# Kernel tuning notes

Hardware: AMD Instinct MI355X
Metric: run time of the kernel (lower is better)

Reference implementation:

```python
import jax, jax.numpy as jnp
import numpy as np

B, S, D, K, F = 4, 2048, 1024, 4, 4096
C_COEF = 8.0  # RG-LRU gating exponent from Griffin paper
EPS = 1e-6


def setup_inputs() -> dict:
    key = jax.random.key(0)
    ks = jax.random.split(key, 12)
    def n(k, shape, scale=1.0):
        return jax.random.normal(k, shape, dtype=jnp.float32) * scale
    sd = 1.0 / np.sqrt(D)
    return {
        "x": n(ks[0], (B, S, D)),
        "velocity": n(ks[1], (B, S, D), 0.1),
        "pre_norm_w": jnp.ones((D,), jnp.float32),
        "conv_kernel": n(ks[2], (D, K), 0.3),   # depthwise causal conv weights
        "conv_bias": jnp.zeros((D,), jnp.float32),
        "W_gate": n(ks[3], (D, D), sd),
        "W_a": n(ks[4], (D, D), sd),
        "lam": n(ks[5], (D,)),
        "W_out": n(ks[6], (2 * D, D), 1.0 / np.sqrt(2 * D)),
        "b_out": jnp.zeros((D,), jnp.float32),
        "log_beta": n(ks[7], (D,), 0.5),
        "ffn_norm_w": jnp.ones((D,), jnp.float32),
        "W_ff1": n(ks[8], (D, F), sd),
        "b_ff1": jnp.zeros((F,), jnp.float32),
        "W_ff2": n(ks[9], (F, D), 1.0 / np.sqrt(F)),
        "b_ff2": jnp.zeros((D,), jnp.float32),
    }


def _rmsnorm(x, w):
    # matches: rsqrt(x.float().pow(2).mean(-1, keepdim=True) + 1e-6); cast back; * weight
    xf = x.astype(jnp.float32)
    rms = jax.lax.rsqrt(jnp.mean(xf * xf, axis=-1, keepdims=True) + EPS)
    return (xf * rms).astype(x.dtype) * w


def _causal_dwconv(x, kernel, bias):
    # y[b,t,d] = bias[d] + sum_k kernel[d,k] * x[b,t-k,d]  (causal depthwise)
    k_taps = kernel.shape[1]
    s = x.shape[1]
    pad = jnp.pad(x, ((0, 0), (k_taps - 1, 0), (0, 0)))
    out = bias
    for k in range(k_taps):  # tiny fixed loop over kernel taps
        out = out + pad[:, k_taps - 1 - k : k_taps - 1 - k + s, :] * kernel[:, k]
    return out


def _griffin_scan(x, W_gate, W_a, lam):
    # RG-LRU: h_t = a_t * h_{t-1} + sqrt(1 - a_t^2) * (i_t * x_t)
    gate = jax.nn.sigmoid(jnp.einsum("bsd,de->bse", x, W_gate))
    log_a = -C_COEF * jax.nn.softplus(lam) * jax.nn.sigmoid(
        jnp.einsum("bsd,de->bse", x, W_a)
    )  # [B,S,D], log_a <= 0
    a = jnp.exp(log_a)
    u = jnp.sqrt(jnp.maximum(1.0 - a * a, 0.0)) * (gate * x)

    def step(h, au):
        a_t, u_t = au
        h = a_t * h + u_t
        return h, h

    a_t = jnp.moveaxis(a, 1, 0)  # [S,B,D]
    u_t = jnp.moveaxis(u, 1, 0)
    h0 = jnp.zeros_like(a_t[0])
    _, hs = jax.lax.scan(step, h0, (a_t, u_t))
    return jnp.moveaxis(hs, 0, 1)  # [B,S,D]


def reference(x, velocity, pre_norm_w, conv_kernel, conv_bias, W_gate, W_a, lam,
              W_out, b_out, log_beta, ffn_norm_w, W_ff1, b_ff1, W_ff2, b_ff2):
    x_norm = _rmsnorm(x, pre_norm_w)
    conv_out = _causal_dwconv(x_norm, conv_kernel, conv_bias)
    griffin_out = _griffin_scan(x_norm, W_gate, W_a, lam)
    mixer_out = jnp.concatenate([conv_out, griffin_out], axis=-1) @ W_out + b_out
    beta = jax.nn.sigmoid(log_beta)
    velocity = beta * velocity + mixer_out
    x = x + velocity
    normed = _rmsnorm(x, ffn_norm_w)
    ffn = jax.nn.gelu(normed @ W_ff1 + b_ff1) @ W_ff2 + b_ff2
    return (x + ffn, velocity)
```

## Files before the change

### kernel.cpp

```cpp
#include <hip/hip_runtime.h>

static constexpr int Bb = 4;
static constexpr int Ss = 2048;
static constexpr int Dd = 1024;
static constexpr int Ff = 4096;
static constexpr int Mm = Bb * Ss;
static constexpr size_t ND = (size_t)Mm * Dd;
static constexpr int CH = 32;
static constexpr int CL = Ss / CH;

typedef __attribute__((ext_vector_type(8))) short short8;
typedef __attribute__((ext_vector_type(4))) float floatx4;

__device__ __forceinline__ unsigned f2bf(float f) {
  unsigned u = __builtin_bit_cast(unsigned, f);
  return (u + 0x7FFFu + ((u >> 16) & 1u)) >> 16;
}
__device__ __forceinline__ float bf2f(unsigned bits) {
  return __builtin_bit_cast(float, bits << 16);
}
__device__ __forceinline__ void gload_lds16(const void* g, void* lds) {
  __builtin_amdgcn_global_load_lds((const __attribute__((address_space(1))) void*)g,
                                   (__attribute__((address_space(3))) void*)lds,
                                   16, 0, 0);
}
__device__ __forceinline__ float fsig(float x) {
  return __builtin_amdgcn_rcpf(1.0f + __expf(-x));
}
__device__ __forceinline__ float fgelu(float v) {
  float z = 1.5957691216057308f * fmaf(0.044715f * v, v * v, v);
  return v * __builtin_amdgcn_rcpf(1.0f + __expf(-z));
}

__global__ __launch_bounds__(256) void wconv_k(const float* __restrict__ W,
                                               unsigned short* __restrict__ WT,
                                               int K, int N) {
  __shared__ float tile[32][33];
  int tx = threadIdx.x & 31, ty = threadIdx.x >> 5;
  int bx = blockIdx.x * 32, by = blockIdx.y * 32;
#pragma unroll
  for (int i = 0; i < 32; i += 8)
    tile[ty + i][tx] = W[(size_t)(by + ty + i) * N + bx + tx];
  __syncthreads();
#pragma unroll
  for (int i = 0; i < 32; i += 8)
    WT[(size_t)(bx + ty + i) * K + by + tx] = (unsigned short)f2bf(tile[tx][ty + i]);
}

__global__ __launch_bounds__(256) void rmsnorm_bf_k(const float* __restrict__ x,
                                                    const float* __restrict__ w,
                                                    unsigned short* __restrict__ out) {
  int row = blockIdx.x;
  const float4* xr = (const float4*)(x + (size_t)row * Dd);
  int t = threadIdx.x;
  float4 v = xr[t];
  float ss = v.x * v.x + v.y * v.y + v.z * v.z + v.w * v.w;
#pragma unroll
  for (int off = 32; off > 0; off >>= 1) ss += __shfl_down(ss, off, 64);
  __shared__ float sb[4];
  if ((t & 63) == 0) sb[t >> 6] = ss;
  __syncthreads();
  float tot = sb[0] + sb[1] + sb[2] + sb[3];
  float sc = rsqrtf(tot * (1.0f / (float)Dd) + 1e-6f);
  float4 wv = ((const float4*)w)[t];
  unsigned lo = f2bf(v.x * sc * wv.x) | (f2bf(v.y * sc * wv.y) << 16);
  unsigned hi = f2bf(v.z * sc * wv.z) | (f2bf(v.w * sc * wv.w) << 16);
  *(uint2*)(out + (size_t)row * Dd + t * 4) = make_uint2(lo, hi);
}

__global__ __launch_bounds__(256) void conv_k(const unsigned short* __restrict__ xn,
                                              const float* __restrict__ kern,
                                              const float* __restrict__ bias,
                                              unsigned short* __restrict__ outC) {
  size_t q = (size_t)blockIdx.x * 256 + threadIdx.x;
  size_t i = q * 4;
  int d = (int)(i & (Dd - 1));
  int m = (int)(i >> 10);
  int t = m & (Ss - 1);
  float acc[4];
#pragma unroll
  for (int j = 0; j < 4; j++) acc[j] = bias[d + j];
#pragma unroll
  for (int k = 0; k < 4; k++) {
    if (t >= k) {
      uint2 xv = *(const uint2*)(xn + i - (size_t)k * Dd);
      float x0 = bf2f(xv.x & 0xFFFF), x1 = bf2f(xv.x >> 16);
      float x2 = bf2f(xv.y & 0xFFFF), x3 = bf2f(xv.y >> 16);
      acc[0] = fmaf(kern[(d + 0) * 4 + k], x0, acc[0]);
      acc[1] = fmaf(kern[(d + 1) * 4 + k], x1, acc[1]);
      acc[2] = fmaf(kern[(d + 2) * 4 + k], x2, acc[2]);
      acc[3] = fmaf(kern[(d + 3) * 4 + k], x3, acc[3]);
    }
  }
  unsigned lo = f2bf(acc[0]) | (f2bf(acc[1]) << 16);
  unsigned hi = f2bf(acc[2]) | (f2bf(acc[3]) << 16);
  *(uint2*)(outC + (size_t)m * (2 * Dd) + d) = make_uint2(lo, hi);
}

template <int MODE>
__global__ __launch_bounds__(512, 2) void bgemm3_k(const unsigned short* __restrict__ A,
                                                   const unsigned short* __restrict__ BT,
                                                   void* __restrict__ Cout,
                                                   int M, int N, int K,
                                                   const float* __restrict__ bias,
                                                   const float* __restrict__ extra,
                                                   const float* __restrict__ vel_in,
                                                   const float* __restrict__ x_in,
                                                   const float* __restrict__ log_beta,
                                                   float* __restrict__ vel_out) {
  __shared__ unsigned short LA[2][256 * 64];
  __shared__ unsigned short LB[2][256 * 64];
  const int tid = threadIdx.x;
  const int wid = tid >> 6, lane = tid & 63;
  const int wm = wid >> 2, wn = wid & 3;
  const int r = lane & 15, quad = lane >> 4, r7 = lane & 7;

  const int gx = gridDim.x;
  int id = blockIdx.y * gx + blockIdx.x;
  const int nwg = gx * gridDim.y;
  id = (id & 7) * (nwg >> 3) + (id >> 3);
  const int bm = (id / gx) * 256, bn = (id % gx) * 256;
  const int NIT = K >> 7;

  const int lrow = lane >> 3;
  const int sblk = (lane & 7) ^ lrow;
  const unsigned short* AsrcB = A  + (size_t)(bm + lrow) * K + sblk * 8;
  const unsigned short* BsrcB = BT + (size_t)(bn + lrow) * K + sblk * 8;

  const int aB = wm * 8192 + r * 64;
  const int bB = wn * 4096 + r * 64;
  const int kq0 = (quad ^ r7) * 8;
  const int kq1 = ((4 + quad) ^ r7) * 8;

  floatx4 acc[8][4];
#pragma unroll
  for (int i = 0; i < 8; i++)
#pragma unroll
    for (int j = 0; j < 4; j++) acc[i][j] = (floatx4){0.f, 0.f, 0.f, 0.f};

#define STG_A(bq, k0, h, s)                                                           \
  gload_lds16(AsrcB + (size_t)((h) * 128 + (s) * 64 + wid * 8) * K + (k0),            \
              (void*)&LA[bq][((h) * 128 + (s) * 64 + wid * 8) * 64])
#define STG_B(bq, k0, h, s)                                                           \
  gload_lds16(BsrcB + (size_t)((h) * 128 + (s) * 64 + wid * 8) * K + (k0),            \
              (void*)&LB[bq][((h) * 128 + (s) * 64 + wid * 8) * 64])
#define RDA(il, IH, buf)                                                              \
  aF[il][0] = *(const short8*)&LA[buf][aB + (IH) * 4096 + (il) * 1024 + kq0];         \
  aF[il][1] = *(const short8*)&LA[buf][aB + (IH) * 4096 + (il) * 1024 + kq1]
#define RDB(BF, jl, jg, buf)                                                          \
  BF[jl][0] = *(const short8*)&LB[buf][bB + (jg) * 1024 + kq0];                       \
  BF[jl][1] = *(const short8*)&LB[buf][bB + (jg) * 1024 + kq1]
#define MM2(il, jl, BF, IH, JH)                                                       \
  acc[(IH) * 4 + (il)][(JH) * 2 + (jl)] = __builtin_amdgcn_mfma_f32_16x16x32_bf16(    \
      BF[jl][0], aF[il][0], acc[(IH) * 4 + (il)][(JH) * 2 + (jl)], 0, 0, 0);          \
  acc[(IH) * 4 + (il)][(JH) * 2 + (jl)] = __builtin_amdgcn_mfma_f32_16x16x32_bf16(    \
      BF[jl][1], aF[il][1], acc[(IH) * 4 + (il)][(JH) * 2 + (jl)], 0, 0, 0)
#define MQUAD(BF, IH, JH)                                                             \
  MM2(0, 0, BF, IH, JH); MM2(0, 1, BF, IH, JH); MM2(1, 0, BF, IH, JH);                \
  MM2(1, 1, BF, IH, JH); MM2(2, 0, BF, IH, JH); MM2(2, 1, BF, IH, JH);                \
  MM2(3, 0, BF, IH, JH); MM2(3, 1, BF, IH, JH)
#define BAR() __builtin_amdgcn_s_barrier()
#define LGK0()                                                                        \
  asm volatile("s_waitcnt lgkmcnt(0)" ::: "memory");                                  \
  __builtin_amdgcn_sched_barrier(0)
#define PRIO(x) __builtin_amdgcn_s_setprio(x)

  STG_A(0, 0, 0, 0); STG_A(0, 0, 0, 1); STG_A(0, 0, 1, 0); STG_A(0, 0, 1, 1);
  STG_B(0, 0, 0, 0); STG_B(0, 0, 0, 1); STG_B(0, 0, 1, 0); STG_B(0, 0, 1, 1);
  STG_B(1, 64, 0, 0); STG_B(1, 64, 0, 1); STG_B(1, 64, 1, 0); STG_B(1, 64, 1, 1);
  asm volatile("s_waitcnt vmcnt(4)" ::: "memory");
  BAR();
  __builtin_amdgcn_sched_barrier(0);

  for (int it = 0; it < NIT; ++it) {
    const int T = 2 * it;
    const int pf = (it + 1 < NIT);
    const int kA1 = (T + 1) << 6;
    const int k2 = (T + 2) << 6, k3 = (T + 3) << 6;
    short8 aF[4][2], b0[2][2], b1[2][2];

    STG_A(1, kA1, 0, 0); STG_A(1, kA1, 0, 1);
    RDA(0, 0, 0); RDA(1, 0, 0); RDA(2, 0, 0); RDA(3, 0, 0);
    RDB(b0, 0, 0, 0); RDB(b0, 1, 1, 0);
    BAR(); LGK0();
    PRIO(1); MQUAD(b0, 0, 0); PRIO(0);
    BAR();

    STG_A(1, kA1, 1, 0); STG_A(1, kA1, 1, 1);
    RDB(b1, 0, 2, 0); RDB(b1, 1, 3, 0);
    BAR(); LGK0();
    PRIO(1); MQUAD(b1, 0, 1); PRIO(0);
    BAR();

    if (pf) { STG_B(0, k2, 0, 0); STG_B(0, k2, 0, 1); }
    RDA(0, 1, 0); RDA(1, 1, 0); RDA(2, 1, 0); RDA(3, 1, 0);
    BAR(); LGK0();
    PRIO(1); MQUAD(b0, 1, 0); PRIO(0);
    BAR();

    if (pf) { STG_B(0, k2, 1, 0); STG_B(0, k2, 1, 1); }
    BAR();
    PRIO(1); MQUAD(b1, 1, 1); PRIO(0);
    if (pf) asm volatile("s_waitcnt vmcnt(4)" ::: "memory");
    else    asm volatile("s_waitcnt vmcnt(0)" ::: "memory");
    BAR();
    __builtin_amdgcn_sched_barrier(0);

    if (pf) { STG_A(0, k2, 0, 0); STG_A(0, k2, 0, 1); }
    RDA(0, 0, 1); RDA(1, 0, 1); RDA(2, 0, 1); RDA(3, 0, 1);
    RDB(b0, 0, 0, 1); RDB(b0, 1, 1, 1);
    BAR(); LGK0();
    PRIO(1); MQUAD(b0, 0, 0); PRIO(0);
    BAR();

    if (pf) { STG_A(0, k2, 1, 0); STG_A(0, k2, 1, 1); }
    RDB(b1, 0, 2, 1); RDB(b1, 1, 3, 1);
    BAR(); LGK0();
    PRIO(1); MQUAD(b1, 0, 1); PRIO(0);
    BAR();

    if (pf) { STG_B(1, k3, 0, 0); STG_B(1, k3, 0, 1); }
    RDA(0, 1, 1); RDA(1, 1, 1); RDA(2, 1, 1); RDA(3, 1, 1);
    BAR(); LGK0();
    PRIO(1); MQUAD(b0, 1, 0); PRIO(0);
    BAR();

    if (pf) { STG_B(1, k3, 1, 0); STG_B(1, k3, 1, 1); }
    BAR();
    PRIO(1); MQUAD(b1, 1, 1); PRIO(0);
    if (pf) {
      asm volatile("s_waitcnt vmcnt(4)" ::: "memory");
      BAR();
      __builtin_amdgcn_sched_barrier(0);
    }
  }
#undef STG_A
#undef STG_B
#undef RDA
#undef RDB
#undef MM2
#undef MQUAD

#pragma unroll
  for (int i = 0; i < 8; i++) {
    int rowg = bm + wm * 128 + i * 16 + r;
#pragma unroll
    for (int j = 0; j < 4; j++) {
      int colg = bn + wn * 64 + j * 16 + quad * 4;
      size_t idx = (size_t)rowg * N + colg;
      float v0 = acc[i][j][0], v1 = acc[i][j][1], v2 = acc[i][j][2], v3 = acc[i][j][3];
      if (MODE & 1) {
        float4 bv = *(const float4*)(bias + colg);
        v0 += bv.x; v1 += bv.y; v2 += bv.z; v3 += bv.w;
      }
      if (MODE & 2) {
        v0 = fgelu(v0); v1 = fgelu(v1); v2 = fgelu(v2); v3 = fgelu(v3);
      }
      if (MODE & 4) {
        float4 ev = *(const float4*)(extra + idx);
        v0 += ev.x; v1 += ev.y; v2 += ev.z; v3 += ev.w;
      }
      if (MODE & 16) {
        float4 lb = *(const float4*)(log_beta + colg);
        float4 vi = *(const float4*)(vel_in + idx);
        float4 xi = *(const float4*)(x_in + idx);
        float4 vn;
        vn.x = fmaf(fsig(lb.x), vi.x, v0);
        vn.y = fmaf(fsig(lb.y), vi.y, v1);
        vn.z = fmaf(fsig(lb.z), vi.z, v2);
        vn.w = fmaf(fsig(lb.w), vi.w, v3);
        *(float4*)(vel_out + idx) = vn;
        v0 = xi.x + vn.x; v1 = xi.y + vn.y; v2 = xi.z + vn.z; v3 = xi.w + vn.w;
      }
      if (MODE & 8) {
        uint2 pk;
        pk.x = f2bf(v0) | (f2bf(v1) << 16);
        pk.y = f2bf(v2) | (f2bf(v3) << 16);
        *(uint2*)((unsigned short*)Cout + idx) = pk;
      } else {
        float4 o; o.x = v0; o.y = v1; o.z = v2; o.w = v3;
        *(float4*)((float*)Cout + idx) = o;
      }
    }
  }
}

template <int MODE>
__global__ __launch_bounds__(512, 2) void bgemm4_k(const unsigned short* __restrict__ A,
                                                   const unsigned short* __restrict__ BT,
                                                   void* __restrict__ Cout,
                                                   int M, int N, int K,
                                                   const float* __restrict__ bias,
                                                   const float* __restrict__ extra,
                                                   const float* __restrict__ vel_in,
                                                   const float* __restrict__ x_in,
                                                   const float* __restrict__ log_beta,
                                                   float* __restrict__ vel_out) {
  __shared__ unsigned short LA[3][256 * 64];
  __shared__ unsigned short LB[2][128 * 64];
  const int tid = threadIdx.x;
  const int wid = tid >> 6, lane = tid & 63;
  const int wm = wid >> 1, wn = wid & 1;
  const int r = lane & 15, quad = lane >> 4, r7 = lane & 7;

  const int gx = gridDim.x;
  int id = blockIdx.y * gx + blockIdx.x;
  const int nwg = gx * gridDim.y;
  id = (id & 7) * (nwg >> 3) + (id >> 3);
  const int bm = (id / gx) * 256, bn = (id % gx) * 128;
  const int NIT = K >> 7;

  const int lrow = lane >> 3;
  const int sblk = (lane & 7) ^ lrow;
  const unsigned short* AsrcB = A  + (size_t)(bm + lrow) * K + sblk * 8;
  const unsigned short* BsrcB = BT + (size_t)(bn + lrow) * K + sblk * 8;

  unsigned short* a0 = &LA[0][0];
  unsigned short* a1 = &LA[1][0];
  unsigned short* a2 = &LA[2][0];
  unsigned short* B0 = &LB[0][0];
  unsigned short* B1 = &LB[1][0];

  const int aB = wm * 4096 + r * 64;
  const int bB = wn * 4096 + r * 64;
  const int kq0 = (quad ^ r7) * 8;
  const int kq1 = ((4 + quad) ^ r7) * 8;

  floatx4 acc[4][4];
#pragma unroll
  for (int i = 0; i < 4; i++)
#pragma unroll
    for (int j = 0; j < 4; j++) acc[i][j] = (floatx4){0.f, 0.f, 0.f, 0.f};

#define STG_A7(dst, k0, h, s)                                                         \
  gload_lds16(AsrcB + (size_t)((h) * 128 + (s) * 64 + wid * 8) * K + (k0),            \
              (void*)((dst) + ((h) * 128 + (s) * 64 + wid * 8) * 64))
#define STG_B7(dst, k0, s)                                                            \
  gload_lds16(BsrcB + (size_t)((s) * 64 + wid * 8) * K + (k0),                        \
              (void*)((dst) + ((s) * 64 + wid * 8) * 64))
#define RDA7(src, IH)                                                                 \
  aF[0][0] = *(const short8*)((src) + aB + (IH) * 2048 + kq0);                        \
  aF[0][1] = *(const short8*)((src) + aB + (IH) * 2048 + kq1);                        \
  aF[1][0] = *(const short8*)((src) + aB + (IH) * 2048 + 1024 + kq0);                 \
  aF[1][1] = *(const short8*)((src) + aB + (IH) * 2048 + 1024 + kq1)
#define RDB7(BF, src, JH)                                                             \
  BF[0][0] = *(const short8*)((src) + bB + (JH) * 2048 + kq0);                        \
  BF[0][1] = *(const short8*)((src) + bB + (JH) * 2048 + kq1);                        \
  BF[1][0] = *(const short8*)((src) + bB + (JH) * 2048 + 1024 + kq0);                 \
  BF[1][1] = *(const short8*)((src) + bB + (JH) * 2048 + 1024 + kq1)
#define MM27(il, jl, BF, IH, JH)                                                      \
  acc[(IH) * 2 + (il)][(JH) * 2 + (jl)] = __builtin_amdgcn_mfma_f32_16x16x32_bf16(    \
      BF[jl][0], aF[il][0], acc[(IH) * 2 + (il)][(JH) * 2 + (jl)], 0, 0, 0);          \
  acc[(IH) * 2 + (il)][(JH) * 2 + (jl)] = __builtin_amdgcn_mfma_f32_16x16x32_bf16(    \
      BF[jl][1], aF[il][1], acc[(IH) * 2 + (il)][(JH) * 2 + (jl)], 0, 0, 0)
#define MQ7(BF, IH, JH)                                                               \
  MM27(0, 0, BF, IH, JH); MM27(0, 1, BF, IH, JH);                                     \
  MM27(1, 0, BF, IH, JH); MM27(1, 1, BF, IH, JH)

  STG_A7(a0, 0, 0, 0); STG_A7(a0, 0, 0, 1); STG_A7(a0, 0, 1, 0); STG_A7(a0, 0, 1, 1);
  STG_B7(B0, 0, 0); STG_B7(B0, 0, 1);
  STG_A7(a1, 64, 0, 0); STG_A7(a1, 64, 0, 1); STG_A7(a1, 64, 1, 0); STG_A7(a1, 64, 1, 1);
  STG_B7(B1, 64, 0); STG_B7(B1, 64, 1);
  asm volatile("s_waitcnt vmcnt(6)" ::: "memory");
  BAR();
  __builtin_amdgcn_sched_barrier(0);

  for (int it = 0; it < NIT; ++it) {
    const int T = 2 * it;
    const int pf = (it + 1 < NIT);
    const int k2 = (T + 2) << 6, k3 = (T + 3) << 6;
    short8 aF[2][2], b0f[2][2], b1f[2][2];

    if (pf) { STG_A7(a2, k2, 0, 0); STG_A7(a2, k2, 0, 1); }
    RDA7(a0, 0); RDB7(b0f, B0, 0);
    BAR(); LGK0();
    PRIO(1); MQ7(b0f, 0, 0); PRIO(0);
    BAR();

    if (pf) { STG_A7(a2, k2, 1, 0); STG_A7(a2, k2, 1, 1); }
    RDB7(b1f, B0, 1);
    BAR(); LGK0();
    PRIO(1); MQ7(b1f, 0, 1); PRIO(0);
    BAR();

    if (pf) STG_B7(B0, k2, 0);
    RDA7(a0, 1);
    BAR(); LGK0();
    PRIO(1); MQ7(b0f, 1, 0); PRIO(0);
    BAR();

    if (pf) STG_B7(B0, k2, 1);
    BAR();
    PRIO(1); MQ7(b1f, 1, 1); PRIO(0);
    if (pf) asm volatile("s_waitcnt vmcnt(6)" ::: "memory");
    else    asm volatile("s_waitcnt vmcnt(0)" ::: "memory");
    BAR();
    __builtin_amdgcn_sched_barrier(0);

    if (pf) { STG_A7(a0, k3, 0, 0); STG_A7(a0, k3, 0, 1); }
    RDA7(a1, 0); RDB7(b0f, B1, 0);
    BAR(); LGK0();
    PRIO(1); MQ7(b0f, 0, 0); PRIO(0);
    BAR();

    if (pf) { STG_A7(a0, k3, 1, 0); STG_A7(a0, k3, 1, 1); }
    RDB7(b1f, B1, 1);
    BAR(); LGK0();
    PRIO(1); MQ7(b1f, 0, 1); PRIO(0);
    BAR();

    if (pf) STG_B7(B1, k3, 0);
    RDA7(a1, 1);
    BAR(); LGK0();
    PRIO(1); MQ7(b0f, 1, 0); PRIO(0);
    BAR();

    if (pf) STG_B7(B1, k3, 1);
    BAR();
    PRIO(1); MQ7(b1f, 1, 1); PRIO(0);
    if (pf) {
      asm volatile("s_waitcnt vmcnt(6)" ::: "memory");
      BAR();
      __builtin_amdgcn_sched_barrier(0);
    }

    unsigned short* tmp = a2; a2 = a1; a1 = a0; a0 = tmp;
  }
#undef STG_A7
#undef STG_B7
#undef RDA7
#undef RDB7
#undef MM27
#undef MQ7
#undef BAR
#undef LGK0
#undef PRIO

#pragma unroll
  for (int i = 0; i < 4; i++) {
    int rowg = bm + wm * 64 + i * 16 + r;
#pragma unroll
    for (int j = 0; j < 4; j++) {
      int colg = bn + wn * 64 + j * 16 + quad * 4;
      size_t idx = (size_t)rowg * N + colg;
      float v0 = acc[i][j][0], v1 = acc[i][j][1], v2 = acc[i][j][2], v3 = acc[i][j][3];
      if (MODE & 1) {
        float4 bv = *(const float4*)(bias + colg);
        v0 += bv.x; v1 += bv.y; v2 += bv.z; v3 += bv.w;
      }
      if (MODE & 2) {
        v0 = fgelu(v0); v1 = fgelu(v1); v2 = fgelu(v2); v3 = fgelu(v3);
      }
      if (MODE & 4) {
        float4 ev = *(const float4*)(extra + idx);
        v0 += ev.x; v1 += ev.y; v2 += ev.z; v3 += ev.w;
      }
      if (MODE & 16) {
        float4 lb = *(const float4*)(log_beta + colg);
        float4 vi = *(const float4*)(vel_in + idx);
        float4 xi = *(const float4*)(x_in + idx);
        float4 vn;
        vn.x = fmaf(fsig(lb.x), vi.x, v0);
        vn.y = fmaf(fsig(lb.y), vi.y, v1);
        vn.z = fmaf(fsig(lb.z), vi.z, v2);
        vn.w = fmaf(fsig(lb.w), vi.w, v3);
        *(float4*)(vel_out + idx) = vn;
        v0 = xi.x + vn.x; v1 = xi.y + vn.y; v2 = xi.z + vn.z; v3 = xi.w + vn.w;
      }
      if (MODE & 8) {
        uint2 pk;
        pk.x = f2bf(v0) | (f2bf(v1) << 16);
        pk.y = f2bf(v2) | (f2bf(v3) << 16);
        *(uint2*)((unsigned short*)Cout + idx) = pk;
      } else {
        float4 o; o.x = v0; o.y = v1; o.z = v2; o.w = v3;
        *(float4*)((float*)Cout + idx) = o;
      }
    }
  }
}

__global__ __launch_bounds__(256) void scan_p1(const unsigned short* __restrict__ gapre,
                                               const unsigned short* __restrict__ xn,
                                               const float* __restrict__ lam,
                                               unsigned short* __restrict__ ub,
                                               float* __restrict__ carryA,
                                               float* __restrict__ carryH) {
  int g = blockIdx.x * 256 + threadIdx.x;
  int e = g & (Dd - 1);
  int bc = g >> 10;
  int b = bc & 3;
  int c = bc >> 2;
  float l = lam[e];
  float sp = fmaxf(l, 0.0f) + log1pf(__expf(-fabsf(l)));
  float m8sp = -8.0f * sp;
  size_t m0 = (size_t)b * Ss + (size_t)c * CL;
  float A = 1.0f, h = 0.0f;
#pragma unroll 4
  for (int t = 0; t < CL; t++) {
    size_t m = m0 + t;
    float gp = bf2f(gapre[m * 2048 + e]);
    float ap = bf2f(gapre[m * 2048 + 1024 + e]);
    float xv = bf2f(xn[m * Dd + e]);
    float a = __expf(m8sp * fsig(ap));
    float u = sqrtf(fmaxf(1.0f - a * a, 0.0f)) * fsig(gp) * xv;
    ub[m * Dd + e] = (unsigned short)f2bf(u);
    A *= a;
    h = fmaf(a, h, u);
  }
  carryA[c * 4096 + b * 1024 + e] = A;
  carryH[c * 4096 + b * 1024 + e] = h;
}

__global__ __launch_bounds__(256) void scan_p2(const float* __restrict__ carryA,
                                               const float* __restrict__ carryH,
                                               float* __restrict__ init) {
  int ch = blockIdx.x * 256 + threadIdx.x;
  float H = 0.0f;
#pragma unroll
  for (int c = 0; c < CH; c++) {
    init[c * 4096 + ch] = H;
    H = fmaf(carryA[c * 4096 + ch], H, carryH[c * 4096 + ch]);
  }
}

__global__ __launch_bounds__(256) void scan_p3(const unsigned short* __restrict__ gapre,
                                               const unsigned short* __restrict__ ub,
                                               const float* __restrict__ lam,
                                               const float* __restrict__ init,
                                               unsigned short* __restrict__ outC) {
  int g = blockIdx.x * 256 + threadIdx.x;
  int e = g & (Dd - 1);
  int bc = g >> 10;
  int b = bc & 3;
  int c = bc >> 2;
  float l = lam[e];
  float sp = fmaxf(l, 0.0f) + log1pf(__expf(-fabsf(l)));
  float m8sp = -8.0f * sp;
  size_t m0 = (size_t)b * Ss + (size_t)c * CL;
  float h = init[c * 4096 + b * 1024 + e];
#pragma unroll 4
  for (int t = 0; t < CL; t++) {
    size_t m = m0 + t;
    float ap = bf2f(gapre[m * 2048 + 1024 + e]);
    float a = __expf(m8sp * fsig(ap));
    float u = bf2f(ub[m * Dd + e]);
    h = fmaf(a, h, u);
    outC[m * (2 * Dd) + Dd + e] = (unsigned short)f2bf(h);
  }
}

extern "C" void kernel_launch(void* const* d_in, const int* in_sizes, int n_in,
                              void* d_out, int out_size, void* d_ws, size_t ws_size,
                              hipStream_t stream) {
  const float* x        = (const float*)d_in[0];
  const float* velocity = (const float*)d_in[1];
  const float* pre_w    = (const float*)d_in[2];
  const float* conv_w   = (const float*)d_in[3];
  const float* conv_b   = (const float*)d_in[4];
  const float* W_gate   = (const float*)d_in[5];
  const float* W_a      = (const float*)d_in[6];
  const float* lam      = (const float*)d_in[7];
  const float* W_out    = (const float*)d_in[8];
  const float* b_out    = (const float*)d_in[9];
  const float* log_beta = (const float*)d_in[10];
  const float* ffn_w    = (const float*)d_in[11];
  const float* W_ff1    = (const float*)d_in[12];
  const float* b_ff1    = (const float*)d_in[13];
  const float* W_ff2    = (const float*)d_in[14];
  const float* b_ff2    = (const float*)d_in[15];

  float* out0 = (float*)d_out;
  float* out1 = out0 + ND;

  const size_t MB = 1024 * 1024;
  char* ws = (char*)d_ws;
  unsigned short* WgaT  = (unsigned short*)ws;
  unsigned short* WoT   = WgaT + (size_t)2 * 1024 * 1024;
  unsigned short* Wf1T  = WoT + (size_t)2 * 1024 * 1024;
  unsigned short* Wf2T  = Wf1T + (size_t)4 * 1024 * 1024;
  float*          mixer = (float*)(ws + 24 * MB);
  float*          carA  = (float*)(ws + 24 * MB);
  float*          carH  = (float*)(ws + 24 * MB + 512 * 1024);
  float*          initb = (float*)(ws + 25 * MB);
  unsigned short* conc  = (unsigned short*)(ws + 56 * MB);
  unsigned short* gapre = (unsigned short*)(ws + 88 * MB);
  unsigned short* xnbf  = (unsigned short*)(ws + 120 * MB);
  unsigned short* ubf   = (unsigned short*)(ws + 136 * MB);
  unsigned short* midbf = (unsigned short*)(ws + 88 * MB);
  unsigned short* nrmbf = (unsigned short*)(ws + 56 * MB);

  const int EB = 256;
  const int egrid4 = (int)(ND / 4 / EB);

  wconv_k<<<dim3(32, 32),  256, 0, stream>>>(W_gate, WgaT, 1024, 1024);
  wconv_k<<<dim3(32, 32),  256, 0, stream>>>(W_a,    WgaT + (size_t)1024 * 1024, 1024, 1024);
  wconv_k<<<dim3(32, 64),  256, 0, stream>>>(W_out,  WoT, 2048, 1024);
  wconv_k<<<dim3(128, 32), 256, 0, stream>>>(W_ff1,  Wf1T, 1024, 4096);
  wconv_k<<<dim3(32, 128), 256, 0, stream>>>(W_ff2,  Wf2T, 4096, 1024);
  rmsnorm_bf_k<<<Mm, 256, 0, stream>>>(x, pre_w, xnbf);
  conv_k<<<egrid4, EB, 0, stream>>>(xnbf, conv_w, conv_b, conc);
  bgemm3_k<8><<<dim3(8, 32), 512, 0, stream>>>(xnbf, WgaT, gapre, Mm, 2048, 1024,
      nullptr, nullptr, nullptr, nullptr, nullptr, nullptr);
  scan_p1<<<512, 256, 0, stream>>>(gapre, xnbf, lam, ubf, carA, carH);
  scan_p2<<<16, 256, 0, stream>>>(carA, carH, initb);
  scan_p3<<<512, 256, 0, stream>>>(gapre, ubf, lam, initb, conc);
  bgemm4_k<1 | 16><<<dim3(8, 32), 512, 0, stream>>>(conc, WoT, mixer, Mm, 1024, 2048,
      b_out, nullptr, velocity, x, log_beta, out1);
  rmsnorm_bf_k<<<Mm, 256, 0, stream>>>(mixer, ffn_w, nrmbf);
  bgemm3_k<1 | 2 | 8><<<dim3(16, 32), 512, 0, stream>>>(nrmbf, Wf1T, midbf, Mm, 4096, 1024,
      b_ff1, nullptr, nullptr, nullptr, nullptr, nullptr);
  bgemm4_k<1 | 4><<<dim3(8, 32), 512, 0, stream>>>(midbf, Wf2T, out0, Mm, 1024, 4096,
      b_ff2, mixer, nullptr, nullptr, nullptr, nullptr);
}
```

Before: 562.3 us.

## Triple-buffer the A tile in LDS with rotating buffer pointers

New measurement: 554.2 us. About the same (-1.4%).

```diff
diff --git a/kernel.cpp b/kernel.cpp
--- a/kernel.cpp
+++ b/kernel.cpp
@@ -108,7 +108,7 @@
                                                    const float* __restrict__ x_in,
                                                    const float* __restrict__ log_beta,
                                                    float* __restrict__ vel_out) {
-  __shared__ unsigned short LA[2][256 * 64];
+  __shared__ unsigned short LA[3][256 * 64];
   __shared__ unsigned short LB[2][256 * 64];
   const int tid = threadIdx.x;
   const int wid = tid >> 6, lane = tid & 63;
@@ -127,6 +127,12 @@
   const unsigned short* AsrcB = A  + (size_t)(bm + lrow) * K + sblk * 8;
   const unsigned short* BsrcB = BT + (size_t)(bn + lrow) * K + sblk * 8;
 
+  unsigned short* a0 = &LA[0][0];
+  unsigned short* a1 = &LA[1][0];
+  unsigned short* a2 = &LA[2][0];
+  unsigned short* Bu0 = &LB[0][0];
+  unsigned short* Bu1 = &LB[1][0];
+
   const int aB = wm * 8192 + r * 64;
   const int bB = wn * 4096 + r * 64;
   const int kq0 = (quad ^ r7) * 8;
@@ -138,18 +144,18 @@
 #pragma unroll
     for (int j = 0; j < 4; j++) acc[i][j] = (floatx4){0.f, 0.f, 0.f, 0.f};
 
-#define STG_A(bq, k0, h, s)                                                           \
+#define STG_A(dst, k0, h, s)                                                          \
   gload_lds16(AsrcB + (size_t)((h) * 128 + (s) * 64 + wid * 8) * K + (k0),            \
-              (void*)&LA[bq][((h) * 128 + (s) * 64 + wid * 8) * 64])
-#define STG_B(bq, k0, h, s)                                                           \
+              (void*)((dst) + ((h) * 128 + (s) * 64 + wid * 8) * 64))
+#define STG_B(dst, k0, h, s)                                                          \
   gload_lds16(BsrcB + (size_t)((h) * 128 + (s) * 64 + wid * 8) * K + (k0),            \
-              (void*)&LB[bq][((h) * 128 + (s) * 64 + wid * 8) * 64])
-#define RDA(il, IH, buf)                                                              \
-  aF[il][0] = *(const short8*)&LA[buf][aB + (IH) * 4096 + (il) * 1024 + kq0];         \
-  aF[il][1] = *(const short8*)&LA[buf][aB + (IH) * 4096 + (il) * 1024 + kq1]
-#define RDB(BF, jl, jg, buf)                                                          \
-  BF[jl][0] = *(const short8*)&LB[buf][bB + (jg) * 1024 + kq0];                       \
-  BF[jl][1] = *(const short8*)&LB[buf][bB + (jg) * 1024 + kq1]
+              (void*)((dst) + ((h) * 128 + (s) * 64 + wid * 8) * 64))
+#define RDA(src, il, IH)                                                              \
+  aF[il][0] = *(const short8*)((src) + aB + (IH) * 4096 + (il) * 1024 + kq0);         \
+  aF[il][1] = *(const short8*)((src) + aB + (IH) * 4096 + (il) * 1024 + kq1)
+#define RDB(BF, src, jl, jg)                                                          \
+  BF[jl][0] = *(const short8*)((src) + bB + (jg) * 1024 + kq0);                       \
+  BF[jl][1] = *(const short8*)((src) + bB + (jg) * 1024 + kq1)
 #define MM2(il, jl, BF, IH, JH)                                                       \
   acc[(IH) * 4 + (il)][(JH) * 2 + (jl)] = __builtin_amdgcn_mfma_f32_16x16x32_bf16(    \
       BF[jl][0], aF[il][0], acc[(IH) * 4 + (il)][(JH) * 2 + (jl)], 0, 0, 0);          \
@@ -165,74 +171,76 @@
   __builtin_amdgcn_sched_barrier(0)
 #define PRIO(x) __builtin_amdgcn_s_setprio(x)
 
-  STG_A(0, 0, 0, 0); STG_A(0, 0, 0, 1); STG_A(0, 0, 1, 0); STG_A(0, 0, 1, 1);
-  STG_B(0, 0, 0, 0); STG_B(0, 0, 0, 1); STG_B(0, 0, 1, 0); STG_B(0, 0, 1, 1);
-  STG_B(1, 64, 0, 0); STG_B(1, 64, 0, 1); STG_B(1, 64, 1, 0); STG_B(1, 64, 1, 1);
-  asm volatile("s_waitcnt vmcnt(4)" ::: "memory");
+  STG_A(a0, 0, 0, 0); STG_A(a0, 0, 0, 1); STG_A(a0, 0, 1, 0); STG_A(a0, 0, 1, 1);
+  STG_B(Bu0, 0, 0, 0); STG_B(Bu0, 0, 0, 1); STG_B(Bu0, 0, 1, 0); STG_B(Bu0, 0, 1, 1);
+  STG_A(a1, 64, 0, 0); STG_A(a1, 64, 0, 1); STG_A(a1, 64, 1, 0); STG_A(a1, 64, 1, 1);
+  STG_B(Bu1, 64, 0, 0); STG_B(Bu1, 64, 0, 1); STG_B(Bu1, 64, 1, 0); STG_B(Bu1, 64, 1, 1);
+  asm volatile("s_waitcnt vmcnt(8)" ::: "memory");
   BAR();
   __builtin_amdgcn_sched_barrier(0);
 
   for (int it = 0; it < NIT; ++it) {
     const int T = 2 * it;
     const int pf = (it + 1 < NIT);
-    const int kA1 = (T + 1) << 6;
     const int k2 = (T + 2) << 6, k3 = (T + 3) << 6;
     short8 aF[4][2], b0[2][2], b1[2][2];
 
-    STG_A(1, kA1, 0, 0); STG_A(1, kA1, 0, 1);
-    RDA(0, 0, 0); RDA(1, 0, 0); RDA(2, 0, 0); RDA(3, 0, 0);
-    RDB(b0, 0, 0, 0); RDB(b0, 1, 1, 0);
+    if (pf) { STG_A(a2, k2, 0, 0); STG_A(a2, k2, 0, 1); }
+    RDA(a0, 0, 0); RDA(a0, 1, 0); RDA(a0, 2, 0); RDA(a0, 3, 0);
+    RDB(b0, Bu0, 0, 0); RDB(b0, Bu0, 1, 1);
     BAR(); LGK0();
     PRIO(1); MQUAD(b0, 0, 0); PRIO(0);
     BAR();
 
-    STG_A(1, kA1, 1, 0); STG_A(1, kA1, 1, 1);
-    RDB(b1, 0, 2, 0); RDB(b1, 1, 3, 0);
+    if (pf) { STG_A(a2, k2, 1, 0); STG_A(a2, k2, 1, 1); }
+    RDB(b1, Bu0, 0, 2); RDB(b1, Bu0, 1, 3);
     BAR(); LGK0();
     PRIO(1); MQUAD(b1, 0, 1); PRIO(0);
     BAR();
 
-    if (pf) { STG_B(0, k2, 0, 0); STG_B(0, k2, 0, 1); }
-    RDA(0, 1, 0); RDA(1, 1, 0); RDA(2, 1, 0); RDA(3, 1, 0);
+    if (pf) { STG_B(Bu0, k2, 0, 0); STG_B(Bu0, k2, 0, 1); }
+    RDA(a0, 0, 1); RDA(a0, 1, 1); RDA(a0, 2, 1); RDA(a0, 3, 1);
     BAR(); LGK0();
     PRIO(1); MQUAD(b0, 1, 0); PRIO(0);
     BAR();
 
-    if (pf) { STG_B(0, k2, 1, 0); STG_B(0, k2, 1, 1); }
+    if (pf) { STG_B(Bu0, k2, 1, 0); STG_B(Bu0, k2, 1, 1); }
     BAR();
     PRIO(1); MQUAD(b1, 1, 1); PRIO(0);
-    if (pf) asm volatile("s_waitcnt vmcnt(4)" ::: "memory");
+    if (pf) asm volatile("s_waitcnt vmcnt(8)" ::: "memory");
     else    asm volatile("s_waitcnt vmcnt(0)" ::: "memory");
     BAR();
     __builtin_amdgcn_sched_barrier(0);
 
-    if (pf) { STG_A(0, k2, 0, 0); STG_A(0, k2, 0, 1); }
-    RDA(0, 0, 1); RDA(1, 0, 1); RDA(2, 0, 1); RDA(3, 0, 1);
-    RDB(b0, 0, 0, 1); RDB(b0, 1, 1, 1);
+    if (pf) { STG_A(a0, k3, 0, 0); STG_A(a0, k3, 0, 1); }
+    RDA(a1, 0, 0); RDA(a1, 1, 0); RDA(a1, 2, 0); RDA(a1, 3, 0);
+    RDB(b0, Bu1, 0, 0); RDB(b0, Bu1, 1, 1);
     BAR(); LGK0();
     PRIO(1); MQUAD(b0, 0, 0); PRIO(0);
     BAR();
 
-    if (pf) { STG_A(0, k2, 1, 0); STG_A(0, k2, 1, 1); }
-    RDB(b1, 0, 2, 1); RDB(b1, 1, 3, 1);
+    if (pf) { STG_A(a0, k3, 1, 0); STG_A(a0, k3, 1, 1); }
+    RDB(b1, Bu1, 0, 2); RDB(b1, Bu1, 1, 3);
     BAR(); LGK0();
     PRIO(1); MQUAD(b1, 0, 1); PRIO(0);
     BAR();
 
-    if (pf) { STG_B(1, k3, 0, 0); STG_B(1, k3, 0, 1); }
-    RDA(0, 1, 1); RDA(1, 1, 1); RDA(2, 1, 1); RDA(3, 1, 1);
+    if (pf) { STG_B(Bu1, k3, 0, 0); STG_B(Bu1, k3, 0, 1); }
+    RDA(a1, 0, 1); RDA(a1, 1, 1); RDA(a1, 2, 1); RDA(a1, 3, 1);
     BAR(); LGK0();
     PRIO(1); MQUAD(b0, 1, 0); PRIO(0);
     BAR();
 
-    if (pf) { STG_B(1, k3, 1, 0); STG_B(1, k3, 1, 1); }
+    if (pf) { STG_B(Bu1, k3, 1, 0); STG_B(Bu1, k3, 1, 1); }
     BAR();
     PRIO(1); MQUAD(b1, 1, 1); PRIO(0);
     if (pf) {
-      asm volatile("s_waitcnt vmcnt(4)" ::: "memory");
+      asm volatile("s_waitcnt vmcnt(8)" ::: "memory");
       BAR();
       __builtin_amdgcn_sched_barrier(0);
     }
+
+    unsigned short* tmp = a2; a2 = a1; a1 = a0; a0 = tmp;
   }
 #undef STG_A
 #undef STG_B
```
